# Kernel tuning notes

Hardware: AMD Instinct MI355X
Metric: run time of the kernel (lower is better)

Reference implementation:

```python
import jax, jax.numpy as jnp
import numpy as np

B, Cin, H, W = 4, 64, 160, 160
Cout, K, STRIDE, PAD = 64, 3, 1, 1
KK = K * K


def setup_inputs() -> dict:
    key = jax.random.key(0)
    ks = jax.random.split(key, 4)
    x = jax.random.normal(ks[0], (B, Cin, H, W), jnp.float32)
    # offset/mask conv params (zero-init in source; small random so offsets are non-trivial)
    offset_w = jax.random.normal(ks[1], (3 * KK, Cin, K, K), jnp.float32) * 0.01
    offset_b = jax.random.normal(ks[2], (3 * KK,), jnp.float32) * 0.01
    fan_in = Cin * K * K
    weight = jax.random.normal(ks[3], (Cout, Cin, K, K), jnp.float32) / np.sqrt(fan_in)
    bias = jnp.zeros((Cout,), jnp.float32)
    return dict(x=x, offset_w=offset_w, offset_b=offset_b, weight=weight, bias=bias)


def _conv2d(x, w, b):
    y = jax.lax.conv_general_dilated(
        x, w, window_strides=(STRIDE, STRIDE),
        padding=[(PAD, PAD), (PAD, PAD)],
        dimension_numbers=('NCHW', 'OIHW', 'NCHW'))
    return y + b[None, :, None, None]


def _deform_conv2d(x, offset, mask, weight, bias):
    # x: [B,C,H,W]; offset: [B,2*KK,Ho,Wo] as (dy,dx) pairs; mask: [B,KK,Ho,Wo]
    Bs, C, Hh, Ww = x.shape
    Ho, Wo = offset.shape[2], offset.shape[3]
    off = offset.reshape(Bs, KK, 2, Ho, Wo)
    dy, dx = off[:, :, 0], off[:, :, 1]            # [B,KK,Ho,Wo]
    ki, kj = jnp.meshgrid(jnp.arange(K), jnp.arange(K), indexing='ij')
    ki = ki.reshape(KK).astype(jnp.float32)
    kj = kj.reshape(KK).astype(jnp.float32)
    hb = (jnp.arange(Ho) * STRIDE - PAD).astype(jnp.float32)
    wb = (jnp.arange(Wo) * STRIDE - PAD).astype(jnp.float32)
    py = dy + ki[None, :, None, None] + hb[None, None, :, None]  # sample y coords
    px = dx + kj[None, :, None, None] + wb[None, None, None, :]  # sample x coords
    y0 = jnp.floor(py); x0 = jnp.floor(px)
    wy1 = py - y0; wy0 = 1.0 - wy1
    wx1 = px - x0; wx0 = 1.0 - wx1
    x_hwc = jnp.transpose(x, (0, 2, 3, 1))          # [B,H,W,C]

    def corner(yc, xc):
        valid = (yc >= 0) & (yc < Hh) & (xc >= 0) & (xc < Ww)
        yi = jnp.clip(yc, 0, Hh - 1).astype(jnp.int32)
        xi = jnp.clip(xc, 0, Ww - 1).astype(jnp.int32)
        g = jax.vmap(lambda img, yy, xx: img[yy, xx])(x_hwc, yi, xi)  # [B,KK,Ho,Wo,C]
        return g * valid[..., None].astype(x.dtype)

    val = (corner(y0, x0) * (wy0 * wx0)[..., None]
           + corner(y0, x0 + 1.0) * (wy0 * wx1)[..., None]
           + corner(y0 + 1.0, x0) * (wy1 * wx0)[..., None]
           + corner(y0 + 1.0, x0 + 1.0) * (wy1 * wx1)[..., None])
    val = val * mask[..., None]                      # modulated (DCNv2)
    w2 = weight.reshape(weight.shape[0], C, KK)      # [O,C,KK]
    out = jnp.einsum('bkhwc,ock->bohw', val, w2)
    return out + bias[None, :, None, None]


def reference(x, offset_w, offset_b, weight, bias):
    out = _conv2d(x, offset_w, offset_b)             # [B,3*KK,Ho,Wo]
    o1, o2, m = jnp.split(out, 3, axis=1)
    offset = jnp.concatenate([o1, o2], axis=1)       # [B,2*KK,Ho,Wo]
    mask = jax.nn.sigmoid(m)
    return _deform_conv2d(x, offset, mask, weight, bias)
```

## Files before the change

### kernel.cpp

```cpp
#include <hip/hip_runtime.h>
#include <math.h>

#define B_ 4
#define CIN 64
#define H_ 160
#define W_ 160
#define COUT 64
#define KK_ 9
#define HW_ (H_ * W_)
#define KTOT 576
#define APITCH 584
#define XPITCH 72
#define SLPITCH 17
#define NTILE 6400
#define TPX   800

typedef __attribute__((ext_vector_type(8))) short bf16x8;
typedef __attribute__((ext_vector_type(4))) float f32x4;

__device__ inline unsigned short f2bf(float f) {
    unsigned int u = __float_as_uint(f);
    u = (u + 0x7FFF + ((u >> 16) & 1)) >> 16;
    return (unsigned short)u;
}

__global__ __launch_bounds__(256) void prep_all_k(const float* __restrict__ x,
                                                  const float* __restrict__ wgt,
                                                  const float* __restrict__ ow,
                                                  float* __restrict__ xt,
                                                  unsigned short* __restrict__ wB,
                                                  unsigned short* __restrict__ wB2) {
    __shared__ float tile[64][33];
    int bid = blockIdx.x;
    int t = threadIdx.x;

    if (bid < 3200) {
        int wt = bid % 5; int tmp = bid / 5;
        int h = tmp % H_; int b = tmp / H_;
        int wbase = wt * 32;

        int w_r = t & 31, c_r = t >> 5;
        const float* xp = x + (size_t)b * CIN * HW_ + (size_t)h * W_ + wbase + w_r;
#pragma unroll
        for (int cl = 0; cl < 8; cl++) {
            int c = cl * 8 + c_r;
            tile[c][w_r] = xp[(size_t)c * HW_];
        }
        __syncthreads();

        int c_w = t & 63, w_w = t >> 6;
        float* op = xt + ((size_t)(b * H_ + h) * W_ + wbase) * 64 + c_w;
#pragma unroll
        for (int wl = 0; wl < 8; wl++) {
            int w = wl * 4 + w_w;
            op[(size_t)w * 64] = tile[c_w][w];
        }
    } else if (bid < 3344) {
        int i = (bid - 3200) * 256 + t;
        int o = i / KTOT, r = i % KTOT;
        int tap = r >> 6, c = r & 63;
        wB[i] = f2bf(wgt[(o * CIN + c) * KK_ + tap]);
    } else {
        int i = (bid - 3344) * 256 + t;
        int n = i / KTOT, r = i % KTOT;
        int tap = r >> 6, c = r & 63;
        wB2[i] = (n < 27) ? f2bf(ow[(n * CIN + c) * KK_ + tap]) : (unsigned short)0;
    }
}

__global__ __launch_bounds__(256, 6) void fused_dcn_k(const float* __restrict__ xt,
                                                      const unsigned short* __restrict__ wB2,
                                                      const float* __restrict__ ob,
                                                      const unsigned short* __restrict__ wB,
                                                      const float* __restrict__ bias,
                                                      float* __restrict__ out) {
    __shared__ __align__(16) char ubuf[16 * APITCH * 2];
    __shared__ __align__(16) char pbuf[144 * 32];
    __shared__ float slog[27 * SLPITCH];
    unsigned short* sX = (unsigned short*)ubuf;
    unsigned short* sA = (unsigned short*)ubuf;
    float4* spar_w = (float4*)pbuf;
    int4*   spar_o = (int4*)(pbuf + 144 * 16);

    int t = threadIdx.x;
    int lane = t & 63, wv = t >> 6;
    int bid = blockIdx.x;
    int tile = (bid & 7) * TPX + (bid >> 3);
    int gp0 = tile * 16;
    int wo0 = gp0 % W_;
    int tmp = gp0 / W_;
    int ho = tmp % H_;
    int b  = tmp / H_;

    const float* xb = xt + (size_t)b * HW_ * 64 + lane;

    for (int i = 0; i < 14; i++) {
        int r = i * 4 + wv;
        if (r < 54) {
            int yy = ho - 1 + r / 18;
            int xx = wo0 - 1 + r % 18;
            float v = 0.f;
            if (yy >= 0 && yy < H_ && xx >= 0 && xx < W_)
                v = xb[(size_t)(yy * W_ + xx) * 64];
            sX[r * XPITCH + lane] = f2bf(v);
        }
    }
    __syncthreads();

    if (wv < 2) {
        int m = lane & 15, q = lane >> 4;
        int oc = wv * 16 + m;
        float bv = (oc < 27) ? ob[oc] : 0.f;
        f32x4 acc = {bv, bv, bv, bv};
        const unsigned short* brow = wB2 + oc * KTOT + q * 8;
#pragma unroll
        for (int kk = 0; kk < 18; kk++) {
            int tap = kk >> 1;
            int row = (tap / 3) * 18 + (tap % 3) + m;
            bf16x8 af = *(const bf16x8*)(sX + row * XPITCH + (kk & 1) * 32 + q * 8);
            bf16x8 bf = *(const bf16x8*)(brow + kk * 32);
            acc = __builtin_amdgcn_mfma_f32_16x16x32_bf16(af, bf, acc, 0, 0, 0);
        }
        if (oc < 27) {
            float* sl = slog + oc * SLPITCH + q * 4;
            if (oc < 18) {
#pragma unroll
                for (int r = 0; r < 4; r++) sl[r] = acc[r];
            } else {
#pragma unroll
                for (int r = 0; r < 4; r++) sl[r] = 1.f / (1.f + expf(-acc[r]));
            }
        }
    }
    __syncthreads();

    if (t < 144) {
        int p = t & 15, k = t >> 4;
        float dyv = slog[(2 * k) * SLPITCH + p];
        float dxv = slog[(2 * k + 1) * SLPITCH + p];
        float mv  = slog[(18 + k) * SLPITCH + p];
        float py = dyv + (float)(k / 3) + (float)(ho - 1);
        float px = dxv + (float)(k % 3) + (float)(wo0 + p - 1);
        float y0f = floorf(py), x0f = floorf(px);
        float wy1 = py - y0f, wx1 = px - x0f;
        float wy0 = 1.f - wy1, wx0 = 1.f - wx1;
        int y0 = (int)y0f, x0 = (int)x0f;
        bool yv0 = (y0 >= 0) && (y0 < H_);
        bool yv1 = (y0 + 1 >= 0) && (y0 + 1 < H_);
        bool xv0 = (x0 >= 0) && (x0 < W_);
        bool xv1 = (x0 + 1 >= 0) && (x0 + 1 < W_);
        float4 w4;
        w4.x = (yv0 && xv0) ? wy0 * wx0 * mv : 0.f;
        w4.y = (yv0 && xv1) ? wy0 * wx1 * mv : 0.f;
        w4.z = (yv1 && xv0) ? wy1 * wx0 * mv : 0.f;
        w4.w = (yv1 && xv1) ? wy1 * wx1 * mv : 0.f;
        spar_w[t] = w4;
        int yc0 = min(max(y0, 0), H_ - 1), yc1 = min(max(y0 + 1, 0), H_ - 1);
        int xc0 = min(max(x0, 0), W_ - 1), xc1 = min(max(x0 + 1, 0), W_ - 1);
        int4 o4;
        o4.x = (yc0 * W_ + xc0) * 64;
        o4.y = (yc0 * W_ + xc1) * 64;
        o4.z = (yc1 * W_ + xc0) * 64;
        o4.w = (yc1 * W_ + xc1) * 64;
        spar_o[t] = o4;
    }
    __syncthreads();

#pragma unroll
    for (int g = 0; g < 9; g++) {
        float4 w4[4]; int4 o4[4];
        float v00[4], v01[4], v10[4], v11[4];
#pragma unroll
        for (int j = 0; j < 4; j++) {
            int task = (g * 4 + j) * 4 + wv;
            w4[j] = spar_w[task];
            o4[j] = spar_o[task];
        }
#pragma unroll
        for (int j = 0; j < 4; j++) {
            v00[j] = xb[o4[j].x];
            v01[j] = xb[o4[j].y];
            v10[j] = xb[o4[j].z];
            v11[j] = xb[o4[j].w];
        }
#pragma unroll
        for (int j = 0; j < 4; j++) {
            int task = (g * 4 + j) * 4 + wv;
            int p = task & 15, k = task >> 4;
            float v = v00[j] * w4[j].x + v01[j] * w4[j].y
                    + v10[j] * w4[j].z + v11[j] * w4[j].w;
            sA[p * APITCH + k * 64 + lane] = f2bf(v);
        }
    }
    __syncthreads();

    int m = lane & 15, q = lane >> 4;
    int o0 = wv * 16 + m;
    float b0 = bias[o0];
    f32x4 acc0 = {b0, b0, b0, b0};
    const unsigned short* arow = sA + m * APITCH + q * 8;
    const unsigned short* br0 = wB + o0 * KTOT + q * 8;
#pragma unroll
    for (int kk = 0; kk < 18; kk++) {
        bf16x8 af  = *(const bf16x8*)(arow + kk * 32);
        bf16x8 bf0 = *(const bf16x8*)(br0 + kk * 32);
        acc0 = __builtin_amdgcn_mfma_f32_16x16x32_bf16(af, bf0, acc0, 0, 0, 0);
    }

    size_t a0 = ((size_t)(b * COUT + o0)) * HW_ + (size_t)ho * W_ + wo0 + q * 4;
    float4 r0; r0.x = acc0[0]; r0.y = acc0[1]; r0.z = acc0[2]; r0.w = acc0[3];
    *(float4*)(out + a0) = r0;
}

extern "C" void kernel_launch(void* const* d_in, const int* in_sizes, int n_in,
                              void* d_out, int out_size, void* d_ws, size_t ws_size,
                              hipStream_t stream) {
    const float* x    = (const float*)d_in[0];
    const float* ow   = (const float*)d_in[1];
    const float* ob   = (const float*)d_in[2];
    const float* wgt  = (const float*)d_in[3];
    const float* bias = (const float*)d_in[4];
    float* out = (float*)d_out;

    float* ws  = (float*)d_ws;
    float* xt  = ws;
    unsigned short* wB  = (unsigned short*)(xt + (size_t)B_ * HW_ * CIN);
    unsigned short* wB2 = wB + (size_t)COUT * KTOT;

    prep_all_k<<<3416, 256, 0, stream>>>(x, wgt, ow, xt, wB, wB2);
    fused_dcn_k<<<NTILE, 256, 0, stream>>>(xt, wB2, ob, wB, bias, out);
}
```

Baseline: 201.7 us.

## Per-wave sampling params, dual MFMA accumulators, wider gather batches in DCN kernel

Each wave now computes bilinear weights and offsets only for the sampling tasks it later consumes. A block-wide barrier can then be replaced by an LDS waitcnt. The gather loop is regrouped into 6 batches of 6 tasks using precomputed byte offsets, so more loads are in flight. Both MFMA chains split into two independent accumulators to shorten dependency chains, and float-to-bf16 uses the HIP intrinsic. These raise register pressure and depend on wave-local LDS visibility being correct.

```diff
diff --git a/kernel.cpp b/kernel.cpp
--- a/kernel.cpp
+++ b/kernel.cpp
@@ -1,4 +1,5 @@
 #include <hip/hip_runtime.h>
+#include <hip/hip_bf16.h>
 #include <math.h>
 
 #define B_ 4
@@ -24,6 +25,13 @@
     return (unsigned short)u;
 }
 
+__device__ inline unsigned short bfc(float f) {
+    __hip_bfloat16 h = __float2bfloat16(f);
+    union { __hip_bfloat16 h; unsigned short u; } cv;
+    cv.h = h;
+    return cv.u;
+}
+
 __global__ __launch_bounds__(256) void prep_all_k(const float* __restrict__ x,
                                                   const float* __restrict__ wgt,
                                                   const float* __restrict__ ow,
@@ -102,7 +110,7 @@
             float v = 0.f;
             if (yy >= 0 && yy < H_ && xx >= 0 && xx < W_)
                 v = xb[(size_t)(yy * W_ + xx) * 64];
-            sX[r * XPITCH + lane] = f2bf(v);
+            sX[r * XPITCH + lane] = bfc(v);
         }
     }
     __syncthreads();
@@ -111,16 +119,22 @@
         int m = lane & 15, q = lane >> 4;
         int oc = wv * 16 + m;
         float bv = (oc < 27) ? ob[oc] : 0.f;
-        f32x4 acc = {bv, bv, bv, bv};
+        f32x4 acc  = {bv, bv, bv, bv};
+        f32x4 acc2 = {0.f, 0.f, 0.f, 0.f};
         const unsigned short* brow = wB2 + oc * KTOT + q * 8;
 #pragma unroll
-        for (int kk = 0; kk < 18; kk++) {
-            int tap = kk >> 1;
+        for (int tap = 0; tap < 9; tap++) {
             int row = (tap / 3) * 18 + (tap % 3) + m;
-            bf16x8 af = *(const bf16x8*)(sX + row * XPITCH + (kk & 1) * 32 + q * 8);
-            bf16x8 bf = *(const bf16x8*)(brow + kk * 32);
-            acc = __builtin_amdgcn_mfma_f32_16x16x32_bf16(af, bf, acc, 0, 0, 0);
-        }
+            const unsigned short* sxr = sX + row * XPITCH + q * 8;
+            bf16x8 af0 = *(const bf16x8*)(sxr);
+            bf16x8 af1 = *(const bf16x8*)(sxr + 32);
+            bf16x8 b0  = *(const bf16x8*)(brow + (2 * tap) * 32);
+            bf16x8 b1  = *(const bf16x8*)(brow + (2 * tap + 1) * 32);
+            acc  = __builtin_amdgcn_mfma_f32_16x16x32_bf16(af0, b0, acc,  0, 0, 0);
+            acc2 = __builtin_amdgcn_mfma_f32_16x16x32_bf16(af1, b1, acc2, 0, 0, 0);
+        }
+#pragma unroll
+        for (int r = 0; r < 4; r++) acc[r] += acc2[r];
         if (oc < 27) {
             float* sl = slog + oc * SLPITCH + q * 4;
             if (oc < 18) {
@@ -134,8 +148,9 @@
     }
     __syncthreads();
 
-    if (t < 144) {
-        int p = t & 15, k = t >> 4;
+    if (lane < 36) {
+        int task = lane * 4 + wv;
+        int p = task & 15, k = task >> 4;
         float dyv = slog[(2 * k) * SLPITCH + p];
         float dxv = slog[(2 * k + 1) * SLPITCH + p];
         float mv  = slog[(18 + k) * SLPITCH + p];
@@ -154,58 +169,64 @@
         w4.y = (yv0 && xv1) ? wy0 * wx1 * mv : 0.f;
         w4.z = (yv1 && xv0) ? wy1 * wx0 * mv : 0.f;
         w4.w = (yv1 && xv1) ? wy1 * wx1 * mv : 0.f;
-        spar_w[t] = w4;
+        spar_w[task] = w4;
         int yc0 = min(max(y0, 0), H_ - 1), yc1 = min(max(y0 + 1, 0), H_ - 1);
         int xc0 = min(max(x0, 0), W_ - 1), xc1 = min(max(x0 + 1, 0), W_ - 1);
         int4 o4;
-        o4.x = (yc0 * W_ + xc0) * 64;
-        o4.y = (yc0 * W_ + xc1) * 64;
-        o4.z = (yc1 * W_ + xc0) * 64;
-        o4.w = (yc1 * W_ + xc1) * 64;
-        spar_o[t] = o4;
-    }
-    __syncthreads();
-
-#pragma unroll
-    for (int g = 0; g < 9; g++) {
-        float4 w4[4]; int4 o4[4];
-        float v00[4], v01[4], v10[4], v11[4];
-#pragma unroll
-        for (int j = 0; j < 4; j++) {
-            int task = (g * 4 + j) * 4 + wv;
-            w4[j] = spar_w[task];
-            o4[j] = spar_o[task];
-        }
-#pragma unroll
-        for (int j = 0; j < 4; j++) {
-            v00[j] = xb[o4[j].x];
-            v01[j] = xb[o4[j].y];
-            v10[j] = xb[o4[j].z];
-            v11[j] = xb[o4[j].w];
-        }
-#pragma unroll
-        for (int j = 0; j < 4; j++) {
-            int task = (g * 4 + j) * 4 + wv;
-            int p = task & 15, k = task >> 4;
-            float v = v00[j] * w4[j].x + v01[j] * w4[j].y
-                    + v10[j] * w4[j].z + v11[j] * w4[j].w;
-            sA[p * APITCH + k * 64 + lane] = f2bf(v);
+        o4.x = (yc0 * W_ + xc0) * 256;
+        o4.y = (yc0 * W_ + xc1) * 256;
+        o4.z = (yc1 * W_ + xc0) * 256;
+        o4.w = (yc1 * W_ + xc1) * 256;
+        spar_o[task] = o4;
+    }
+    __asm__ volatile("s_waitcnt lgkmcnt(0)" ::: "memory");
+
+    {
+        unsigned lane4 = (unsigned)lane << 2;
+        const char* xu = (const char*)xt + (size_t)b * ((size_t)HW_ * 64 * 4);
+#pragma unroll
+        for (int g = 0; g < 6; g++) {
+            float v00[6], v01[6], v10[6], v11[6];
+#pragma unroll
+            for (int j = 0; j < 6; j++) {
+                int task = (g * 6 + j) * 4 + wv;
+                int4 o4 = spar_o[task];
+                v00[j] = *(const float*)(xu + ((unsigned)o4.x + lane4));
+                v01[j] = *(const float*)(xu + ((unsigned)o4.y + lane4));
+                v10[j] = *(const float*)(xu + ((unsigned)o4.z + lane4));
+                v11[j] = *(const float*)(xu + ((unsigned)o4.w + lane4));
+            }
+#pragma unroll
+            for (int j = 0; j < 6; j++) {
+                int task = (g * 6 + j) * 4 + wv;
+                float4 w4 = spar_w[task];
+                int p = task & 15, k = task >> 4;
+                float v = v00[j] * w4.x + v01[j] * w4.y
+                        + v10[j] * w4.z + v11[j] * w4.w;
+                sA[p * APITCH + k * 64 + lane] = bfc(v);
+            }
         }
     }
     __syncthreads();
 
     int m = lane & 15, q = lane >> 4;
     int o0 = wv * 16 + m;
-    float b0 = bias[o0];
-    f32x4 acc0 = {b0, b0, b0, b0};
+    float b0v = bias[o0];
+    f32x4 acc0 = {b0v, b0v, b0v, b0v};
+    f32x4 acc1 = {0.f, 0.f, 0.f, 0.f};
     const unsigned short* arow = sA + m * APITCH + q * 8;
     const unsigned short* br0 = wB + o0 * KTOT + q * 8;
 #pragma unroll
-    for (int kk = 0; kk < 18; kk++) {
-        bf16x8 af  = *(const bf16x8*)(arow + kk * 32);
-        bf16x8 bf0 = *(const bf16x8*)(br0 + kk * 32);
-        acc0 = __builtin_amdgcn_mfma_f32_16x16x32_bf16(af, bf0, acc0, 0, 0, 0);
-    }
+    for (int tap = 0; tap < 9; tap++) {
+        bf16x8 af0 = *(const bf16x8*)(arow + (2 * tap) * 32);
+        bf16x8 af1 = *(const bf16x8*)(arow + (2 * tap + 1) * 32);
+        bf16x8 b0  = *(const bf16x8*)(br0 + (2 * tap) * 32);
+        bf16x8 b1  = *(const bf16x8*)(br0 + (2 * tap + 1) * 32);
+        acc0 = __builtin_amdgcn_mfma_f32_16x16x32_bf16(af0, b0, acc0, 0, 0, 0);
+        acc1 = __builtin_amdgcn_mfma_f32_16x16x32_bf16(af1, b1, acc1, 0, 0, 0);
+    }
+#pragma unroll
+    for (int r = 0; r < 4; r++) acc0[r] += acc1[r];
 
     size_t a0 = ((size_t)(b * COUT + o0)) * HW_ + (size_t)ho * W_ + wo0 + q * 4;
     float4 r0; r0.x = acc0[0]; r0.y = acc0[1]; r0.z = acc0[2]; r0.w = acc0[3];
```

Result: no change. 201.7 us (+0.0%).
